# Kernel tuning notes

Hardware: AMD Instinct MI355X
Metric: run time of the kernel (lower is better)

Reference implementation:

```python
import jax, jax.numpy as jnp
import numpy as np

T_TYPES = 3
B = 4096
NUM_ALLY = 10
NUM_OPP = 11
D_IN = 64
D_HID = 64
NEG_INF = -1000000.0


def setup_inputs() -> dict:
    key = jax.random.key(0)
    k1, k2, k3, k4 = jax.random.split(key, 4)
    n_nodes = 1 + NUM_ALLY + NUM_OPP
    h = jax.random.normal(k1, (B, n_nodes, D_IN), dtype=jnp.float32)
    mask = jax.random.randint(k2, (T_TYPES, B, n_nodes), 0, 2).astype(bool)
    # kaiming-ish scaling so attention logits are in a sane range
    W = jax.random.normal(k3, (T_TYPES, D_IN, D_HID), dtype=jnp.float32) / np.sqrt(D_IN).astype(np.float32)
    a = jax.random.normal(k4, (T_TYPES, 2 * D_HID, 1), dtype=jnp.float32) / np.sqrt(2 * D_HID).astype(np.float32)
    return {"h": h, "num_ally": NUM_ALLY, "num_opp": NUM_OPP, "ALL_TYPE_MASK": mask, "W": W, "a": a}


def reference(h, num_ally, num_opp, ALL_TYPE_MASK, W, a):
    T = W.shape[0]
    Hd = W.shape[2]
    Bb = h.shape[0]

    mask_self = ALL_TYPE_MASK[:, :, 0:1]                    # [T,B,1]
    mask_ally = ALL_TYPE_MASK[:, :, 1:1 + num_ally]         # [T,B,Na]
    mask_opp = ALL_TYPE_MASK[:, :, 1 + num_ally:]           # [T,B,No]
    h_self = h[:, 0:1, :]
    h_ally = h[:, 1:1 + num_ally, :]
    h_opp = h[:, 1 + num_ally:, :]

    # per-type projections: [T,B,n,H]
    H_SELF = jnp.einsum('bnd,tdh->tbnh', h_self, W)
    H_ALLY = jnp.einsum('bnd,tdh->tbnh', h_ally, W)
    H_OPP = jnp.einsum('bnd,tdh->tbnh', h_opp, W)

    def branch(Hn, maskn, n):
        # Hn: [T,B,n,H] neighbor features projected by each type's W
        # cartesian product over (self-type s, neighbor-type t)
        self_b = jnp.broadcast_to(H_SELF[:, None], (T, T, Bb, n, Hd))   # [s,t,B,n,H]
        nb = jnp.broadcast_to(Hn[None], (T, T, Bb, n, Hd))              # [s,t,B,n,H]
        inp = jnp.concatenate([self_b, nb], axis=-1)                    # [s,t,B,n,2H]
        # attention vector a indexed by neighbor-type t (as in the torch loop)
        e = jnp.einsum('stbnc,tc->stbn', inp, a[..., 0])                # [s,t,B,n]
        e = e.transpose(2, 0, 1, 3).reshape(Bb, T * T * n)              # [B, T*T*n]
        m = jnp.broadcast_to(maskn[None], (T, T, Bb, n)).transpose(2, 0, 1, 3).reshape(Bb, T * T * n)
        e = jnp.where(m, NEG_INF, e)
        attn = jax.nn.softmax(e, axis=-1)
        attn = jnp.where(m, 0.0, attn)
        Hflat = nb.transpose(2, 0, 1, 3, 4).reshape(Bb, T * T * n, Hd)
        return jnp.einsum('bk,bkh->bh', attn, Hflat)                    # [B,H]

    ally_sum = branch(H_ALLY, mask_ally, num_ally)
    opp_sum = branch(H_OPP, mask_opp, num_opp)

    # self features gated by self-type mask, summed over types: [B,H]
    h_self_sum = (H_SELF * mask_self[..., None].astype(H_SELF.dtype)).sum(axis=0)[:, 0, :]

    H_E = jax.nn.elu(h_self_sum + ally_sum + opp_sum)
    return H_E.reshape(Bb, Hd)
```

## Files before the change

### kernel.cpp

```cpp
#include <hip/hip_runtime.h>
#include <math.h>

#define BATCH   4096
#define NN      22
#define D       64
#define NEG_BIG (-3.0e38f)

#define WAVES   8
#define NB      2
#define BPB     (WAVES * NB)
#define GRID    (BATCH / BPB)
#define THREADS (WAVES * 64)

#define WT_OFF   0
#define WT_T     4352
#define UV_OFF   13056
#define UV_ROW   68
#define H_OFF    13872
#define H_WAVE   1496
#define H_ROW    68
#define G_OFF    25840
#define G_SEG    192
#define W_OFF    28912
#define W_SEG    96
#define LDS_FLOATS 29680
#define LDS_BYTES  (LDS_FLOATS * 4)

__device__ __forceinline__ float wave_sum(float x) {
#pragma unroll
    for (int m = 32; m >= 1; m >>= 1) x += __shfl_xor(x, m, 64);
    return x;
}
__device__ __forceinline__ float wave_max(float x) {
#pragma unroll
    for (int m = 32; m >= 1; m >>= 1) x = fmaxf(x, __shfl_xor(x, m, 64));
    return x;
}
__device__ __forceinline__ float dot4(float4 p, float4 q) {
    return p.x * q.x + p.y * q.y + p.z * q.z + p.w * q.w;
}

__global__ __launch_bounds__(THREADS, 1)
void hetgat_kernel(const float* __restrict__ h,
                   const void* __restrict__ mask_raw,
                   const float* __restrict__ W,
                   const float* __restrict__ a,
                   float* __restrict__ out) {
    extern __shared__ float lds[];

    const int tid  = threadIdx.x;
    const int lane = tid & 63;
    const int wave = tid >> 6;

#pragma unroll
    for (int i = 0; i < 24; ++i) {
        int e  = i * 512 + tid;
        int t  = e >> 12;
        int r  = e & 4095;
        int d  = r >> 6, hd = r & 63;
        lds[WT_OFF + t * WT_T + hd * 68 + d] = W[e];
    }
#pragma unroll
    for (int k = 0; k < 2; ++k) {
        int e = k * 512 + tid;
        if (e < 768) {
            int vec = e >> 6, d = e & 63;
            int s    = (vec < 9) ? (vec / 3) : (vec - 9);
            int aoff = (vec < 9) ? ((vec % 3) * 2 * D) : ((vec - 9) * 2 * D + D);
            const float4* wrow = (const float4*)(W + (size_t)s * 4096 + d * 64);
            const float4* arow = (const float4*)(a + aoff);
            float acc = 0.f;
#pragma unroll
            for (int i = 0; i < 16; ++i) acc += dot4(wrow[i], arow[i]);
            lds[UV_OFF + vec * UV_ROW + d] = acc;
        }
    }
    __syncthreads();

    const unsigned char* mb = (const unsigned char*)mask_raw;
    const bool bytelayout = (__ballot(((lane & 3) != 0) && (mb[lane] != 0)) != 0ULL);

    float* hW    = lds + H_OFF + wave * H_WAVE;
    float* wwave = lds + W_OFF + wave * W_SEG;

    int tq = lane / 21; if (tq > 2) tq = 2;
    int nn = lane - tq * 21 + 1;
    int row = (nn > 21) ? 21 : nn;
    const bool valid = (lane < 63);

#pragma unroll
    for (int nb = 0; nb < NB; ++nb) {
        const int b = blockIdx.x * BPB + wave * NB + nb;
        const float* hb = h + (size_t)b * NN * D;

#pragma unroll
        for (int k = 0; k < 6; ++k) {
            int f4 = k * 64 + lane;
            if (f4 < 352) {
                float4 v = ((const float4*)hb)[f4];
                int f = f4 * 4;
                int n = f >> 6, c = f & 63;
                *(float4*)&hW[n * H_ROW + c] = v;
            }
        }
        __threadfence_block();

        float hreg[NN];
#pragma unroll
        for (int n = 0; n < NN; ++n) hreg[n] = hW[n * H_ROW + lane];

        unsigned long long mt[3];
        if (bytelayout) {
#pragma unroll
            for (int t = 0; t < 3; ++t)
                mt[t] = __ballot((lane < NN) && (mb[(size_t)t * BATCH * NN + (size_t)b * NN + lane] != 0));
        } else {
            const int* mi = (const int*)mask_raw;
#pragma unroll
            for (int t = 0; t < 3; ++t)
                mt[t] = __ballot((lane < NN) && (mi[(size_t)t * BATCH * NN + (size_t)b * NN + lane] != 0));
        }

        float zacc = 0.f;
        {
            const float4* hr = (const float4*)&hW[row * H_ROW];
            const float4* vr = (const float4*)&lds[UV_OFF + (9 + tq) * UV_ROW];
#pragma unroll
            for (int i = 0; i < 16; ++i) zacc += dot4(hr[i], vr[i]);
        }

        float eacc = 0.f;
        if (lane < 9) {
            const float4* h0 = (const float4*)&hW[0];
            const float4* ur = (const float4*)&lds[UV_OFF + lane * UV_ROW];
#pragma unroll
            for (int i = 0; i < 16; ++i) eacc += dot4(h0[i], ur[i]);
        }
        float E0 = __shfl(eacc, 0 + tq, 64);
        float E1 = __shfl(eacc, 3 + tq, 64);
        float E2 = __shfl(eacc, 6 + tq, 64);
        float Em = fmaxf(fmaxf(E0, E1), E2);
        float Sv = __expf(E0 - Em) + __expf(E1 - Em) + __expf(E2 - Em);

        float val = zacc + Em;
        bool  msk = (mt[tq] >> nn) & 1ull;
        bool  fa  = valid && (nn <= 10) && !msk;
        bool  fo  = valid && (nn >= 11) && !msk;

        float Ma = wave_max(fa ? val : NEG_BIG);
        float Mo = wave_max(fo ? val : NEG_BIG);

        float ca = fa ? __expf(val - Ma) * Sv : 0.f;
        float co = fo ? __expf(val - Mo) * Sv : 0.f;
        float Da = wave_sum(ca);
        float Do = wave_sum(co);
        float rDa = (Da > 0.f) ? 1.0f / Da : 0.f;
        float rDo = (Do > 0.f) ? 1.0f / Do : 0.f;

        float w = fa ? ca * rDa : (fo ? co * rDo : 0.f);

        wwave[tq * 24 + (nn - 1)] = w;
        __threadfence_block();

        float gt[3];
#pragma unroll
        for (int t = 0; t < 3; ++t) {
            gt[t] = ((mt[t] >> 0) & 1ull) ? hreg[0] : 0.f;
#pragma unroll
            for (int j = 0; j < 5; ++j) {
                float4 w4 = *(const float4*)&wwave[t * 24 + 4 * j];
                gt[t] += w4.x * hreg[1 + 4 * j] + w4.y * hreg[2 + 4 * j]
                       + w4.z * hreg[3 + 4 * j] + w4.w * hreg[4 + 4 * j];
            }
            gt[t] += wwave[t * 24 + 20] * hreg[21];
        }

        float* gW = lds + G_OFF + (wave * NB + nb) * G_SEG;
#pragma unroll
        for (int t = 0; t < 3; ++t) gW[t * 64 + lane] = gt[t];
    }
    __threadfence_block();

    float res[NB];
#pragma unroll
    for (int nb = 0; nb < NB; ++nb) res[nb] = 0.f;

    const float4* g0 = (const float4*)(lds + G_OFF + (wave * NB + 0) * G_SEG);
    const float4* g1 = (const float4*)(lds + G_OFF + (wave * NB + 1) * G_SEG);
#pragma unroll
    for (int t = 0; t < 3; ++t) {
        const float4* wr = (const float4*)&lds[WT_OFF + t * WT_T + lane * 68];
#pragma unroll
        for (int i = 0; i < 16; ++i) {
            float4 wv  = wr[i];
            float4 ga4 = g0[t * 16 + i];
            float4 gb4 = g1[t * 16 + i];
            res[0] += dot4(ga4, wv);
            res[1] += dot4(gb4, wv);
        }
    }

#pragma unroll
    for (int nb = 0; nb < NB; ++nb) {
        const int b = blockIdx.x * BPB + wave * NB + nb;
        float x = res[nb];
        float y = (x > 0.f) ? x : (__expf(x) - 1.0f);
        out[(size_t)b * D + lane] = y;
    }
}

extern "C" void kernel_launch(void* const* d_in, const int* in_sizes, int n_in,
                              void* d_out, int out_size, void* d_ws, size_t ws_size,
                              hipStream_t stream) {
    const float* h    = (const float*)d_in[0];
    const void*  mask = d_in[3];
    const float* W    = (const float*)d_in[4];
    const float* a    = (const float*)d_in[5];
    float*       out  = (float*)d_out;

    hipFuncSetAttribute((const void*)hetgat_kernel,
                        hipFuncAttributeMaxDynamicSharedMemorySize, LDS_BYTES);
    hetgat_kernel<<<GRID, THREADS, LDS_BYTES, stream>>>(h, mask, W, a, out);
}
```

Baseline: 93.09 us.

## Restructure to one batch row per wave with split-K final projection

After: 123.6 us. +32.8%, slower.

```diff
diff --git a/kernel.cpp b/kernel.cpp
--- a/kernel.cpp
+++ b/kernel.cpp
@@ -4,26 +4,19 @@
 #define BATCH   4096
 #define NN      22
 #define D       64
-#define NEG_BIG (-3.0e38f)
 
-#define WAVES   8
-#define NB      2
-#define BPB     (WAVES * NB)
+#define WAVES   16
+#define THREADS 1024
+#define BPB     16
 #define GRID    (BATCH / BPB)
-#define THREADS (WAVES * 64)
 
-#define WT_OFF   0
-#define WT_T     4352
-#define UV_OFF   13056
+#define W_OFF    0
+#define UV_OFF   12288
 #define UV_ROW   68
-#define H_OFF    13872
-#define H_WAVE   1496
-#define H_ROW    68
-#define G_OFF    25840
-#define G_SEG    192
-#define W_OFF    28912
-#define W_SEG    96
-#define LDS_FLOATS 29680
+#define WSC_OFF  13104
+#define G_OFF    14640
+#define P_OFF    17712
+#define LDS_FLOATS 21808
 #define LDS_BYTES  (LDS_FLOATS * 4)
 
 __device__ __forceinline__ float wave_sum(float x) {
@@ -31,16 +24,15 @@
     for (int m = 32; m >= 1; m >>= 1) x += __shfl_xor(x, m, 64);
     return x;
 }
-__device__ __forceinline__ float wave_max(float x) {
-#pragma unroll
-    for (int m = 32; m >= 1; m >>= 1) x = fmaxf(x, __shfl_xor(x, m, 64));
-    return x;
-}
 __device__ __forceinline__ float dot4(float4 p, float4 q) {
     return p.x * q.x + p.y * q.y + p.z * q.z + p.w * q.w;
 }
+__device__ __forceinline__ void lds_fence_wave() {
+    asm volatile("s_waitcnt lgkmcnt(0)" ::: "memory");
+    __builtin_amdgcn_sched_barrier(0);
+}
 
-__global__ __launch_bounds__(THREADS, 1)
+__global__ __launch_bounds__(THREADS)
 void hetgat_kernel(const float* __restrict__ h,
                    const void* __restrict__ mask_raw,
                    const float* __restrict__ W,
@@ -52,160 +44,140 @@
     const int lane = tid & 63;
     const int wave = tid >> 6;
 
+    {
+        const float4* Wg4 = (const float4*)W;
+        float4*       Wl4 = (float4*)(lds + W_OFF);
 #pragma unroll
-    for (int i = 0; i < 24; ++i) {
-        int e  = i * 512 + tid;
-        int t  = e >> 12;
-        int r  = e & 4095;
-        int d  = r >> 6, hd = r & 63;
-        lds[WT_OFF + t * WT_T + hd * 68 + d] = W[e];
+        for (int k = 0; k < 3; ++k) Wl4[tid + k * 1024] = Wg4[tid + k * 1024];
     }
+    if (tid < 768) {
+        int vec = tid >> 6, d = tid & 63;
+        int s    = (vec < 9) ? (vec / 3) : (vec - 9);
+        int aoff = (vec < 9) ? ((vec % 3) * 128) : ((vec - 9) * 128 + 64);
+        const float4* wrow = (const float4*)(W + (size_t)s * 4096 + d * 64);
+        const float4* arow = (const float4*)(a + aoff);
+        float acc = 0.f;
 #pragma unroll
-    for (int k = 0; k < 2; ++k) {
-        int e = k * 512 + tid;
-        if (e < 768) {
-            int vec = e >> 6, d = e & 63;
-            int s    = (vec < 9) ? (vec / 3) : (vec - 9);
-            int aoff = (vec < 9) ? ((vec % 3) * 2 * D) : ((vec - 9) * 2 * D + D);
-            const float4* wrow = (const float4*)(W + (size_t)s * 4096 + d * 64);
-            const float4* arow = (const float4*)(a + aoff);
-            float acc = 0.f;
-#pragma unroll
-            for (int i = 0; i < 16; ++i) acc += dot4(wrow[i], arow[i]);
-            lds[UV_OFF + vec * UV_ROW + d] = acc;
-        }
+        for (int i = 0; i < 16; ++i) acc += dot4(wrow[i], arow[i]);
+        lds[UV_OFF + vec * UV_ROW + d] = acc;
     }
     __syncthreads();
 
     const unsigned char* mb = (const unsigned char*)mask_raw;
     const bool bytelayout = (__ballot(((lane & 3) != 0) && (mb[lane] != 0)) != 0ULL);
 
-    float* hW    = lds + H_OFF + wave * H_WAVE;
-    float* wwave = lds + W_OFF + wave * W_SEG;
+    const int b = blockIdx.x * BPB + wave;
+    const float* hb = h + (size_t)b * NN * D;
+
+    float hreg[NN];
+#pragma unroll
+    for (int n = 0; n < NN; ++n) hreg[n] = hb[n * D + lane];
+
+    unsigned long long mt[3];
+    if (bytelayout) {
+#pragma unroll
+        for (int t = 0; t < 3; ++t)
+            mt[t] = __ballot((lane < NN) && (mb[(size_t)t * BATCH * NN + (size_t)b * NN + lane] != 0));
+    } else {
+        const int* mi = (const int*)mask_raw;
+#pragma unroll
+        for (int t = 0; t < 3; ++t)
+            mt[t] = __ballot((lane < NN) && (mi[(size_t)t * BATCH * NN + (size_t)b * NN + lane] != 0));
+    }
 
     int tq = lane / 21; if (tq > 2) tq = 2;
-    int nn = lane - tq * 21 + 1;
-    int row = (nn > 21) ? 21 : nn;
+    int nn_ = lane - tq * 21 + 1;
+    int row = (nn_ > 21) ? 21 : nn_;
     const bool valid = (lane < 63);
 
+    float zacc = 0.f;
+    {
+        const float4* hr = (const float4*)(hb + row * D);
+        const float4* vr = (const float4*)&lds[UV_OFF + (9 + tq) * UV_ROW];
 #pragma unroll
-    for (int nb = 0; nb < NB; ++nb) {
-        const int b = blockIdx.x * BPB + wave * NB + nb;
-        const float* hb = h + (size_t)b * NN * D;
+        for (int i = 0; i < 16; ++i) zacc += dot4(hr[i], vr[i]);
+    }
+
+    float eacc = 0.f;
+    if (lane < 9) {
+        const float4* h0 = (const float4*)hb;
+        const float4* ur = (const float4*)&lds[UV_OFF + lane * UV_ROW];
+#pragma unroll
+        for (int i = 0; i < 16; ++i) eacc += dot4(h0[i], ur[i]);
+    }
+    float E0 = __shfl(eacc, 0 + tq, 64);
+    float E1 = __shfl(eacc, 3 + tq, 64);
+    float E2 = __shfl(eacc, 6 + tq, 64);
+    float Se = __expf(E0) + __expf(E1) + __expf(E2);
+
+    bool msk = (mt[tq] >> nn_) & 1ull;
+    bool fa  = valid && (nn_ <= 10) && !msk;
+    bool fo  = valid && (nn_ >= 11) && !msk;
+    float coef = (fa || fo) ? __expf(fminf(zacc, 60.f)) * Se : 0.f;
+    float ca = fa ? coef : 0.f;
+    float co = fo ? coef : 0.f;
+    float Da = wave_sum(ca);
+    float Do = wave_sum(co);
+    float rDa = (Da > 0.f) ? 1.0f / Da : 0.f;
+    float rDo = (Do > 0.f) ? 1.0f / Do : 0.f;
+    float wv  = fa ? ca * rDa : (fo ? co * rDo : 0.f);
+
+    lds[WSC_OFF + wave * 96 + tq * 32 + (nn_ - 1)] = wv;
+    lds_fence_wave();
 
 #pragma unroll
-        for (int k = 0; k < 6; ++k) {
-            int f4 = k * 64 + lane;
-            if (f4 < 352) {
-                float4 v = ((const float4*)hb)[f4];
-                int f = f4 * 4;
-                int n = f >> 6, c = f & 63;
-                *(float4*)&hW[n * H_ROW + c] = v;
+    for (int t = 0; t < 3; ++t) {
+        float gt = ((mt[t] >> 0) & 1ull) ? hreg[0] : 0.f;
+        const int base = WSC_OFF + wave * 96 + t * 32;
+#pragma unroll
+        for (int j = 0; j < 5; ++j) {
+            float4 w4 = *(const float4*)&lds[base + 4 * j];
+            gt += w4.x * hreg[1 + 4 * j] + w4.y * hreg[2 + 4 * j]
+                + w4.z * hreg[3 + 4 * j] + w4.w * hreg[4 + 4 * j];
+        }
+        gt += lds[base + 20] * hreg[21];
+        lds[G_OFF + wave * 192 + t * 64 + lane] = gt;
+    }
+    __syncthreads();
+
+    {
+        const int bg = wave & 3, dq = wave >> 2;
+        const int b0 = bg * 4;
+        float acc0 = 0.f, acc1 = 0.f, acc2 = 0.f, acc3 = 0.f;
+#pragma unroll
+        for (int t = 0; t < 3; ++t) {
+#pragma unroll
+            for (int i = 0; i < 4; ++i) {
+                const int d = dq * 16 + i * 4;
+                float w0 = lds[W_OFF + t * 4096 + (d + 0) * 64 + lane];
+                float w1 = lds[W_OFF + t * 4096 + (d + 1) * 64 + lane];
+                float w2 = lds[W_OFF + t * 4096 + (d + 2) * 64 + lane];
+                float w3 = lds[W_OFF + t * 4096 + (d + 3) * 64 + lane];
+                float4 g0 = *(const float4*)&lds[G_OFF + (b0 + 0) * 192 + t * 64 + d];
+                float4 g1 = *(const float4*)&lds[G_OFF + (b0 + 1) * 192 + t * 64 + d];
+                float4 g2 = *(const float4*)&lds[G_OFF + (b0 + 2) * 192 + t * 64 + d];
+                float4 g3 = *(const float4*)&lds[G_OFF + (b0 + 3) * 192 + t * 64 + d];
+                acc0 += g0.x * w0 + g0.y * w1 + g0.z * w2 + g0.w * w3;
+                acc1 += g1.x * w0 + g1.y * w1 + g1.z * w2 + g1.w * w3;
+                acc2 += g2.x * w0 + g2.y * w1 + g2.z * w2 + g2.w * w3;
+                acc3 += g3.x * w0 + g3.y * w1 + g3.z * w2 + g3.w * w3;
             }
         }
-        __threadfence_block();
+        lds[P_OFF + dq * 1024 + (b0 + 0) * 64 + lane] = acc0;
+        lds[P_OFF + dq * 1024 + (b0 + 1) * 64 + lane] = acc1;
+        lds[P_OFF + dq * 1024 + (b0 + 2) * 64 + lane] = acc2;
+        lds[P_OFF + dq * 1024 + (b0 + 3) * 64 + lane] = acc3;
+    }
+    __syncthreads();
 
-        float hreg[NN];
-#pragma unroll
-        for (int n = 0; n < NN; ++n) hreg[n] = hW[n * H_ROW + lane];
-
-        unsigned long long mt[3];
-        if (bytelayout) {
-#pragma unroll
-            for (int t = 0; t < 3; ++t)
-                mt[t] = __ballot((lane < NN) && (mb[(size_t)t * BATCH * NN + (size_t)b * NN + lane] != 0));
-        } else {
-            const int* mi = (const int*)mask_raw;
-#pragma unroll
-            for (int t = 0; t < 3; ++t)
-                mt[t] = __ballot((lane < NN) && (mi[(size_t)t * BATCH * NN + (size_t)b * NN + lane] != 0));
-        }
-
-        float zacc = 0.f;
-        {
-            const float4* hr = (const float4*)&hW[row * H_ROW];
-            const float4* vr = (const float4*)&lds[UV_OFF + (9 + tq) * UV_ROW];
-#pragma unroll
-            for (int i = 0; i < 16; ++i) zacc += dot4(hr[i], vr[i]);
-        }
-
-        float eacc = 0.f;
-        if (lane < 9) {
-            const float4* h0 = (const float4*)&hW[0];
-            const float4* ur = (const float4*)&lds[UV_OFF + lane * UV_ROW];
-#pragma unroll
-            for (int i = 0; i < 16; ++i) eacc += dot4(h0[i], ur[i]);
-        }
-        float E0 = __shfl(eacc, 0 + tq, 64);
-        float E1 = __shfl(eacc, 3 + tq, 64);
-        float E2 = __shfl(eacc, 6 + tq, 64);
-        float Em = fmaxf(fmaxf(E0, E1), E2);
-        float Sv = __expf(E0 - Em) + __expf(E1 - Em) + __expf(E2 - Em);
-
-        float val = zacc + Em;
-        bool  msk = (mt[tq] >> nn) & 1ull;
-        bool  fa  = valid && (nn <= 10) && !msk;
-        bool  fo  = valid && (nn >= 11) && !msk;
-
-        float Ma = wave_max(fa ? val : NEG_BIG);
-        float Mo = wave_max(fo ? val : NEG_BIG);
-
-        float ca = fa ? __expf(val - Ma) * Sv : 0.f;
-        float co = fo ? __expf(val - Mo) * Sv : 0.f;
-        float Da = wave_sum(ca);
-        float Do = wave_sum(co);
-        float rDa = (Da > 0.f) ? 1.0f / Da : 0.f;
-        float rDo = (Do > 0.f) ? 1.0f / Do : 0.f;
-
-        float w = fa ? ca * rDa : (fo ? co * rDo : 0.f);
-
-        wwave[tq * 24 + (nn - 1)] = w;
-        __threadfence_block();
-
-        float gt[3];
-#pragma unroll
-        for (int t = 0; t < 3; ++t) {
-            gt[t] = ((mt[t] >> 0) & 1ull) ? hreg[0] : 0.f;
-#pragma unroll
-            for (int j = 0; j < 5; ++j) {
-                float4 w4 = *(const float4*)&wwave[t * 24 + 4 * j];
-                gt[t] += w4.x * hreg[1 + 4 * j] + w4.y * hreg[2 + 4 * j]
-                       + w4.z * hreg[3 + 4 * j] + w4.w * hreg[4 + 4 * j];
-            }
-            gt[t] += wwave[t * 24 + 20] * hreg[21];
-        }
-
-        float* gW = lds + G_OFF + (wave * NB + nb) * G_SEG;
-#pragma unroll
-        for (int t = 0; t < 3; ++t) gW[t * 64 + lane] = gt[t];
-    }
-    __threadfence_block();
-
-    float res[NB];
-#pragma unroll
-    for (int nb = 0; nb < NB; ++nb) res[nb] = 0.f;
-
-    const float4* g0 = (const float4*)(lds + G_OFF + (wave * NB + 0) * G_SEG);
-    const float4* g1 = (const float4*)(lds + G_OFF + (wave * NB + 1) * G_SEG);
-#pragma unroll
-    for (int t = 0; t < 3; ++t) {
-        const float4* wr = (const float4*)&lds[WT_OFF + t * WT_T + lane * 68];
-#pragma unroll
-        for (int i = 0; i < 16; ++i) {
-            float4 wv  = wr[i];
-            float4 ga4 = g0[t * 16 + i];
-            float4 gb4 = g1[t * 16 + i];
-            res[0] += dot4(ga4, wv);
-            res[1] += dot4(gb4, wv);
-        }
-    }
-
-#pragma unroll
-    for (int nb = 0; nb < NB; ++nb) {
-        const int b = blockIdx.x * BPB + wave * NB + nb;
-        float x = res[nb];
-        float y = (x > 0.f) ? x : (__expf(x) - 1.0f);
-        out[(size_t)b * D + lane] = y;
+    {
+        const int p2 = tid >> 6;
+        float s = lds[P_OFF + 0 * 1024 + p2 * 64 + lane]
+                + lds[P_OFF + 1 * 1024 + p2 * 64 + lane]
+                + lds[P_OFF + 2 * 1024 + p2 * 64 + lane]
+                + lds[P_OFF + 3 * 1024 + p2 * 64 + lane];
+        float y = (s > 0.f) ? s : (__expf(s) - 1.0f);
+        out[(size_t)(blockIdx.x * BPB + p2) * D + lane] = y;
     }
 }
 
```
